# Kernel optimization log

Measured on AMD Instinct MI355X. Metric: run time of the kernel, lower is better.

Reference implementation:

```python
import jax, jax.numpy as jnp
import numpy as np

N = 131072      # number of RoIs (instances)
D = 1024        # in_channels
H = 1024        # hidden dim (hard-coded in module)
L = 4           # number of FPN levels / routed experts
STD = 0.01      # init std for all weights (biases zero)


def setup_inputs() -> dict:
    key = jax.random.key(0)
    k = jax.random.split(key, 5)
    x = jax.random.normal(k[0], (N, D), dtype=jnp.float32)
    levels = jax.random.randint(k[1], (N,), 0, L, dtype=jnp.int32)
    # Per-level MLP params, normal(std=0.01) weights, zero biases.
    W1 = jax.random.normal(k[2], (L, D, H), dtype=jnp.float32) * STD
    b1 = jnp.zeros((L, H), dtype=jnp.float32)
    W2 = jax.random.normal(k[3], (L, H, H), dtype=jnp.float32) * STD
    b2 = jnp.zeros((L, H), dtype=jnp.float32)
    W3 = jax.random.normal(k[4], (L, H, 1), dtype=jnp.float32) * STD
    b3 = jnp.zeros((L, 1), dtype=jnp.float32)
    return {"x": x, "levels": levels, "W1": W1, "b1": b1,
            "W2": W2, "b2": b2, "W3": W3, "b3": b3}


def reference(x, levels, W1, b1, W2, b2, W3, b3):
    # Hard-routed per-level 3-layer MLP (FC-ReLU x2 + FC), dropout in eval
    # mode (identity). Rows routed to level l get that level's MLP output;
    # implemented jit-compatibly with a fixed loop over the 4 levels and a
    # row mask instead of data-dependent gather/scatter.
    result = jnp.zeros((x.shape[0], 1), dtype=x.dtype)
    for lvl in range(L):
        h = jax.nn.relu(x @ W1[lvl] + b1[lvl])       # [N, H]
        h = jax.nn.relu(h @ W2[lvl] + b2[lvl])       # [N, H]
        out = h @ W3[lvl] + b3[lvl]                  # [N, 1]
        result = jnp.where((levels == lvl)[:, None], out, result)
    return result
```

## Files before the change

### kernel.cpp

```cpp
#include <hip/hip_runtime.h>

#define NROWS   131072
#define KDIM    1024
#define NLVL    4
#define SLOT_CAP 131584
#define NSB     1028

#define OFF_IDX  1024ull
#define OFF_PART (OFF_IDX + (size_t)SLOT_CAP * 4)
#define OFF_WT1  (OFF_PART + (size_t)SLOT_CAP * 64)
#define OFF_WT2  (OFF_WT1 + 8388608ull)
#define OFF_XBF  (OFF_WT2 + 8388608ull)
#define OFF_H1   (OFF_XBF + 268435456ull)

typedef __bf16 bf16x8 __attribute__((ext_vector_type(8)));
typedef float f32x4 __attribute__((ext_vector_type(4)));
typedef unsigned short u16x4 __attribute__((ext_vector_type(4)));

__device__ __forceinline__ unsigned short f2bf(float f) {
  unsigned int u = __float_as_uint(f);
  u += 0x7fffu + ((u >> 16) & 1u);
  return (unsigned short)(u >> 16);
}

__device__ __forceinline__ void gld_lds16(const void* g, void* l) {
  __builtin_amdgcn_global_load_lds(
      (const __attribute__((address_space(1))) void*)g,
      (__attribute__((address_space(3))) void*)l, 16, 0, 0);
}


__global__ void k_hist(const int* __restrict__ levels, int n, int* __restrict__ meta) {
  __shared__ int h[NLVL];
  if (threadIdx.x < NLVL) h[threadIdx.x] = 0;
  __syncthreads();
  for (int t = blockIdx.x * blockDim.x + threadIdx.x; t < n; t += gridDim.x * blockDim.x)
    atomicAdd(&h[levels[t]], 1);
  __syncthreads();
  if (threadIdx.x < NLVL) atomicAdd(&meta[threadIdx.x], h[threadIdx.x]);
}

__global__ void k_seg(int* meta) {
  if (threadIdx.x == 0 && blockIdx.x == 0) {
    int s = 0;
    for (int l = 0; l < NLVL; ++l) {
      int pc = (meta[l] + 127) & ~127;
      meta[8 + l] = s;
      meta[12 + l] = pc;
      s += pc;
    }
  }
}

__global__ void k_scatter(const int* __restrict__ levels, int n,
                          int* __restrict__ meta, int* __restrict__ idx) {
  __shared__ int h[NLVL], base[NLVL], cur[NLVL];
  int t = blockIdx.x * blockDim.x + threadIdx.x;
  if (threadIdx.x < NLVL) { h[threadIdx.x] = 0; cur[threadIdx.x] = 0; }
  __syncthreads();
  int lvl = 0;
  if (t < n) { lvl = levels[t]; atomicAdd(&h[lvl], 1); }
  __syncthreads();
  if (threadIdx.x < NLVL)
    base[threadIdx.x] = atomicAdd(&meta[4 + threadIdx.x], h[threadIdx.x]);
  __syncthreads();
  if (t < n) {
    int p = atomicAdd(&cur[lvl], 1);
    idx[meta[8 + lvl] + base[lvl] + p] = t;
  }
}

__global__ void k_cvt_x(const f32x4* __restrict__ x, u16x4* __restrict__ xb, int n4) {
  for (int t = blockIdx.x * blockDim.x + threadIdx.x; t < n4; t += gridDim.x * blockDim.x) {
    f32x4 v = x[t];
    u16x4 o;
    o[0] = f2bf(v[0]); o[1] = f2bf(v[1]); o[2] = f2bf(v[2]); o[3] = f2bf(v[3]);
    xb[t] = o;
  }
}

__global__ void k_twt(const float* __restrict__ W, unsigned short* __restrict__ Wt) {
  __shared__ float tile[32][33];
  int lvl = blockIdx.z;
  int k0 = blockIdx.x * 32, n0 = blockIdx.y * 32;
  int tx = threadIdx.x, ty = threadIdx.y;
  const float* Wp = W + (size_t)lvl * 1048576;
  unsigned short* Wtp = Wt + (size_t)lvl * 1048576;
#pragma unroll
  for (int i = 0; i < 4; ++i)
    tile[ty + i * 8][tx] = Wp[(size_t)(k0 + ty + i * 8) * 1024 + n0 + tx];
  __syncthreads();
#pragma unroll
  for (int i = 0; i < 4; ++i) {
    int nn = ty + i * 8;
    Wtp[(size_t)(n0 + nn) * 1024 + k0 + tx] = f2bf(tile[tx][nn]);
  }
}

template <int PASS>
__global__ __launch_bounds__(256) void k_gemm(
    const unsigned short* __restrict__ Asrc,
    const unsigned short* __restrict__ Wt,
    const float* __restrict__ bias,
    const float* __restrict__ w3,
    const int* __restrict__ meta,
    const int* __restrict__ idx,
    unsigned short* __restrict__ hout,
    float* __restrict__ partial) {
  const int bid = blockIdx.x;
  const int swz = (bid & 7) * NSB + (bid >> 3);
  const int nb = swz & 7;
  const int sb = swz >> 3;

  const int slotbase = sb * 128;
  if (slotbase >= meta[11] + meta[15]) return;
  int lvl;
  if      (slotbase < meta[9])  lvl = 0;
  else if (slotbase < meta[10]) lvl = 1;
  else if (slotbase < meta[11]) lvl = 2;
  else                          lvl = 3;

  const int tid = threadIdx.x;
  const int ln = tid & 63;
  const int w = tid >> 6;
  const int wm = w >> 1, wn = w & 1;

  __shared__ unsigned short Xl[128 * 64];
  __shared__ unsigned short Wl[128 * 64];

  const int srow = ln >> 3;
  const int schk = (ln & 7) ^ srow;
  const unsigned short* ag[4];
  const unsigned short* wg[4];
  unsigned short* xd[4];
  unsigned short* wd[4];
#pragma unroll
  for (int j = 0; j < 4; ++j) {
    int rloc = w * 32 + j * 8 + srow;
    int arow = (PASS == 1) ? idx[slotbase + rloc] : (slotbase + rloc);
    ag[j] = Asrc + (size_t)arow * 1024 + schk * 8;
    wg[j] = Wt + ((size_t)lvl * 1024 + nb * 128 + rloc) * 1024 + schk * 8;
    xd[j] = &Xl[(w * 32 + j * 8) * 64];
    wd[j] = &Wl[(w * 32 + j * 8) * 64];
  }

  const f32x4 vzero = {0.f, 0.f, 0.f, 0.f};
  f32x4 acc[4][4];
#pragma unroll
  for (int a = 0; a < 4; ++a)
#pragma unroll
    for (int b = 0; b < 4; ++b) acc[a][b] = vzero;

  const int rx = ln & 7;
  const int kg = ln >> 4;

  for (int k0 = 0; k0 < KDIM; k0 += 64) {
    __syncthreads();
#pragma unroll
    for (int j = 0; j < 4; ++j) gld_lds16(ag[j] + k0, xd[j]);
#pragma unroll
    for (int j = 0; j < 4; ++j) gld_lds16(wg[j] + k0, wd[j]);
    __syncthreads();
#pragma unroll
    for (int kk = 0; kk < 64; kk += 32) {
      const int chk = (((kk >> 3) + kg) ^ rx) * 8;
      bf16x8 aop[4], bop[4];
#pragma unroll
      for (int nf = 0; nf < 4; ++nf)
        aop[nf] = *(const bf16x8*)&Wl[(wn * 64 + nf * 16 + (ln & 15)) * 64 + chk];
#pragma unroll
      for (int mf = 0; mf < 4; ++mf)
        bop[mf] = *(const bf16x8*)&Xl[(wm * 64 + mf * 16 + (ln & 15)) * 64 + chk];
#pragma unroll
      for (int nf = 0; nf < 4; ++nf)
#pragma unroll
        for (int mf = 0; mf < 4; ++mf)
          acc[nf][mf] = __builtin_amdgcn_mfma_f32_16x16x32_bf16(aop[nf], bop[mf], acc[nf][mf], 0, 0, 0);
    }
  }

  const float* bv = bias + lvl * 1024;
  const int m_lo = ln & 15, n_lo = (ln >> 4) * 4;

  if (PASS == 1) {
#pragma unroll
    for (int nf = 0; nf < 4; ++nf) {
#pragma unroll
      for (int mf = 0; mf < 4; ++mf) {
        int slot = slotbase + wm * 64 + mf * 16 + m_lo;
        int col = nb * 128 + wn * 64 + nf * 16 + n_lo;
        f32x4 bb = *(const f32x4*)&bv[col];
        f32x4 v = acc[nf][mf];
        u16x4 o;
#pragma unroll
        for (int r = 0; r < 4; ++r) {
          float f = v[r] + bb[r];
          f = fmaxf(f, 0.f);
          o[r] = f2bf(f);
        }
        *(u16x4*)&hout[(size_t)slot * 1024 + col] = o;
      }
    }
  } else {
    const float* w3v = w3 + lvl * 1024;
    float ps[4] = {0.f, 0.f, 0.f, 0.f};
#pragma unroll
    for (int mf = 0; mf < 4; ++mf) {
#pragma unroll
      for (int nf = 0; nf < 4; ++nf) {
        int col = nb * 128 + wn * 64 + nf * 16 + n_lo;
        f32x4 bb = *(const f32x4*)&bv[col];
        f32x4 ww = *(const f32x4*)&w3v[col];
        f32x4 v = acc[nf][mf];
#pragma unroll
        for (int r = 0; r < 4; ++r) {
          float f = fmaxf(v[r] + bb[r], 0.f);
          ps[mf] += f * ww[r];
        }
      }
    }
#pragma unroll
    for (int mf = 0; mf < 4; ++mf) {
      float p = ps[mf];
      p += __shfl_xor(p, 16);
      p += __shfl_xor(p, 32);
      if (ln < 16) {
        int slot = slotbase + wm * 64 + mf * 16 + ln;
        partial[(size_t)slot * 16 + nb * 2 + wn] = p;
      }
    }
  }
}

__global__ void k_final(const int* __restrict__ meta, const int* __restrict__ idx,
                        const float* __restrict__ partial, const float* __restrict__ b3,
                        float* __restrict__ out) {
  int t = blockIdx.x * blockDim.x + threadIdx.x;
  int total = meta[11] + meta[15];
  if (t >= total) return;
  int lvl;
  if (t < meta[9]) lvl = 0;
  else if (t < meta[10]) lvl = 1;
  else if (t < meta[11]) lvl = 2;
  else lvl = 3;
  int local = t - meta[8 + lvl];
  if (local >= meta[lvl]) return;
  int row = idx[t];
  const float* pp = partial + (size_t)t * 16;
  float s = 0.f;
#pragma unroll
  for (int j = 0; j < 16; ++j) s += pp[j];
  out[row] = s + b3[lvl];
}

extern "C" void kernel_launch(void* const* d_in, const int* in_sizes, int n_in,
                              void* d_out, int out_size, void* d_ws, size_t ws_size,
                              hipStream_t stream) {
  const float* x      = (const float*)d_in[0];
  const int*   levels = (const int*)d_in[1];
  const float* W1     = (const float*)d_in[2];
  const float* b1     = (const float*)d_in[3];
  const float* W2     = (const float*)d_in[4];
  const float* b2     = (const float*)d_in[5];
  const float* W3     = (const float*)d_in[6];
  const float* b3     = (const float*)d_in[7];
  float* out = (float*)d_out;

  char* ws = (char*)d_ws;
  int* meta = (int*)ws;
  int* idx = (int*)(ws + OFF_IDX);
  float* partial = (float*)(ws + OFF_PART);
  unsigned short* Wt1 = (unsigned short*)(ws + OFF_WT1);
  unsigned short* Wt2 = (unsigned short*)(ws + OFF_WT2);
  unsigned short* xb  = (unsigned short*)(ws + OFF_XBF);
  unsigned short* h1  = (unsigned short*)(ws + OFF_H1);

  hipMemsetAsync(d_ws, 0, OFF_IDX + (size_t)SLOT_CAP * 4, stream);
  k_hist<<<256, 256, 0, stream>>>(levels, NROWS, meta);
  k_seg<<<1, 64, 0, stream>>>(meta);
  k_scatter<<<512, 256, 0, stream>>>(levels, NROWS, meta, idx);
  k_cvt_x<<<2048, 256, 0, stream>>>((const f32x4*)x, (u16x4*)xb, NROWS * (KDIM / 4));
  k_twt<<<dim3(32, 32, 4), dim3(32, 8), 0, stream>>>(W1, Wt1);
  k_twt<<<dim3(32, 32, 4), dim3(32, 8), 0, stream>>>(W2, Wt2);

  k_gemm<1><<<8 * NSB, 256, 0, stream>>>(xb, Wt1, b1, nullptr, meta, idx, h1, nullptr);
  k_gemm<2><<<8 * NSB, 256, 0, stream>>>(h1, Wt2, b2, W3, meta, idx, nullptr, partial);

  k_final<<<514, 256, 0, stream>>>(meta, idx, partial, b3, out);
}
```

Baseline: 960.1 us.

## Use 256x256 tiles with double-buffered 8-wave pipelined GEMM schedule

Enlarges the GEMM tile to 256x256 with 512 threads and a 128KB LDS double buffer, and moves level padding to 256 rows. The main loop is rewritten as an explicit software pipeline that interleaves async global-to-LDS loads with MFMA phases, using barriers, waitcnt and setprio. The aim is higher data reuse per load and overlap of memory traffic with matrix math. In exchange it uses heavy LDS and registers, lowering occupancy, and adds more padding rows per level.

```diff
diff --git a/kernel.cpp b/kernel.cpp
--- a/kernel.cpp
+++ b/kernel.cpp
@@ -3,8 +3,8 @@
 #define NROWS   131072
 #define KDIM    1024
 #define NLVL    4
-#define SLOT_CAP 131584
-#define NSB     1028
+#define SLOT_CAP 132096
+#define NSB     516
 
 #define OFF_IDX  1024ull
 #define OFF_PART (OFF_IDX + (size_t)SLOT_CAP * 4)
@@ -44,7 +44,7 @@
   if (threadIdx.x == 0 && blockIdx.x == 0) {
     int s = 0;
     for (int l = 0; l < NLVL; ++l) {
-      int pc = (meta[l] + 127) & ~127;
+      int pc = (meta[l] + 255) & ~255;
       meta[8 + l] = s;
       meta[12 + l] = pc;
       s += pc;
@@ -97,8 +97,23 @@
   }
 }
 
+#define BARR __builtin_amdgcn_s_barrier()
+#define WAIT_L  asm volatile("s_waitcnt lgkmcnt(0)" ::: "memory")
+#define WAIT_V6 asm volatile("s_waitcnt vmcnt(6) lgkmcnt(0)" ::: "memory")
+#define PRIO(x) __builtin_amdgcn_s_setprio(x)
+
+#define RD_W(pi,kk) { const char* p_ = lds + (((pi)*4 + (kk)) << 14) + offW0; \
+  wf[0] = *(const bf16x8*)(p_);        wf[1] = *(const bf16x8*)(p_ + 1024);  \
+  wf[2] = *(const bf16x8*)(p_ + 2048); wf[3] = *(const bf16x8*)(p_ + 3072); }
+#define RD_X(pi,kk,mh) { const char* p_ = lds + (((pi)*4 + 2 + (kk)) << 14) + offX0 + (mh)*4096; \
+  xf[0] = *(const bf16x8*)(p_);        xf[1] = *(const bf16x8*)(p_ + 1024);  \
+  xf[2] = *(const bf16x8*)(p_ + 2048); xf[3] = *(const bf16x8*)(p_ + 3072); }
+#define MMA(mh) { _Pragma("unroll") for (int nf_ = 0; nf_ < 4; ++nf_) { \
+  _Pragma("unroll") for (int j_ = 0; j_ < 4; ++j_) \
+    acc[nf_][(mh)*4 + j_] = __builtin_amdgcn_mfma_f32_16x16x32_bf16(wf[nf_], xf[j_], acc[nf_][(mh)*4 + j_], 0, 0, 0); } }
+
 template <int PASS>
-__global__ __launch_bounds__(256) void k_gemm(
+__global__ __launch_bounds__(512, 2) void k_gemm(
     const unsigned short* __restrict__ Asrc,
     const unsigned short* __restrict__ Wt,
     const float* __restrict__ bias,
@@ -107,12 +122,13 @@
     const int* __restrict__ idx,
     unsigned short* __restrict__ hout,
     float* __restrict__ partial) {
+  __shared__ __align__(16) char lds[131072];
+
   const int bid = blockIdx.x;
-  const int swz = (bid & 7) * NSB + (bid >> 3);
-  const int nb = swz & 7;
-  const int sb = swz >> 3;
-
-  const int slotbase = sb * 128;
+  const int swz = (bid & 7) * (NSB * 4 / 8) + (bid >> 3);
+  const int nb = swz & 3;
+  const int sb = swz >> 2;
+  const int slotbase = sb * 256;
   if (slotbase >= meta[11] + meta[15]) return;
   int lvl;
   if      (slotbase < meta[9])  lvl = 0;
@@ -121,112 +137,111 @@
   else                          lvl = 3;
 
   const int tid = threadIdx.x;
-  const int ln = tid & 63;
-  const int w = tid >> 6;
-  const int wm = w >> 1, wn = w & 1;
-
-  __shared__ unsigned short Xl[128 * 64];
-  __shared__ unsigned short Wl[128 * 64];
-
-  const int srow = ln >> 3;
-  const int schk = (ln & 7) ^ srow;
-  const unsigned short* ag[4];
-  const unsigned short* wg[4];
-  unsigned short* xd[4];
-  unsigned short* wd[4];
-#pragma unroll
-  for (int j = 0; j < 4; ++j) {
-    int rloc = w * 32 + j * 8 + srow;
-    int arow = (PASS == 1) ? idx[slotbase + rloc] : (slotbase + rloc);
-    ag[j] = Asrc + (size_t)arow * 1024 + schk * 8;
-    wg[j] = Wt + ((size_t)lvl * 1024 + nb * 128 + rloc) * 1024 + schk * 8;
-    xd[j] = &Xl[(w * 32 + j * 8) * 64];
-    wd[j] = &Wl[(w * 32 + j * 8) * 64];
-  }
+  const int ln  = tid & 63;
+  const int w   = tid >> 6;
+  const int wn  = w & 3;
+  const int wm  = w >> 2;
+  const int l15 = ln & 15;
+
+  const int rr0 = w * 16 + (ln >> 2);
+  const int cch = (ln & 3) ^ ((rr0 >> 1) & 3);
+  int ar0, ar1;
+  if (PASS == 1) { ar0 = idx[slotbase + rr0]; ar1 = idx[slotbase + rr0 + 128]; }
+  else           { ar0 = slotbase + rr0;      ar1 = slotbase + rr0 + 128; }
+  const char* xs0 = (const char*)Asrc + (size_t)ar0 * 2048 + cch * 16;
+  const char* xs1 = (const char*)Asrc + (size_t)ar1 * 2048 + cch * 16;
+  const char* wlv = (const char*)Wt + ((size_t)lvl << 21);
+  const char* ws0 = wlv + (size_t)(nb * 256 + rr0) * 2048 + cch * 16;
+  const char* ws1 = ws0 + 128 * 2048;
+
+  auto STG = [&](int t, int isX, int kkh) {
+    char* db = (char*)lds + (((t & 1) * 4 + isX * 2 + kkh) << 14) + (w << 10);
+    const char* s0 = isX ? xs0 : ws0;
+    const char* s1 = isX ? xs1 : ws1;
+    const int o = t * 128 + kkh * 64;
+    gld_lds16(s0 + o, db);
+    gld_lds16(s1 + o, db + 8192);
+  };
+
+  const int xorc  = ((ln >> 4) ^ ((l15 >> 1) & 3)) * 16;
+  const int offW0 = (wn * 64 + l15) * 64 + xorc;
+  const int offX0 = (wm * 128 + l15) * 64 + xorc;
 
   const f32x4 vzero = {0.f, 0.f, 0.f, 0.f};
-  f32x4 acc[4][4];
+  f32x4 acc[4][8];
 #pragma unroll
   for (int a = 0; a < 4; ++a)
 #pragma unroll
-    for (int b = 0; b < 4; ++b) acc[a][b] = vzero;
-
-  const int rx = ln & 7;
-  const int kg = ln >> 4;
-
-  for (int k0 = 0; k0 < KDIM; k0 += 64) {
-    __syncthreads();
-#pragma unroll
-    for (int j = 0; j < 4; ++j) gld_lds16(ag[j] + k0, xd[j]);
-#pragma unroll
-    for (int j = 0; j < 4; ++j) gld_lds16(wg[j] + k0, wd[j]);
-    __syncthreads();
-#pragma unroll
-    for (int kk = 0; kk < 64; kk += 32) {
-      const int chk = (((kk >> 3) + kg) ^ rx) * 8;
-      bf16x8 aop[4], bop[4];
-#pragma unroll
-      for (int nf = 0; nf < 4; ++nf)
-        aop[nf] = *(const bf16x8*)&Wl[(wn * 64 + nf * 16 + (ln & 15)) * 64 + chk];
-#pragma unroll
-      for (int mf = 0; mf < 4; ++mf)
-        bop[mf] = *(const bf16x8*)&Xl[(wm * 64 + mf * 16 + (ln & 15)) * 64 + chk];
-#pragma unroll
-      for (int nf = 0; nf < 4; ++nf)
-#pragma unroll
-        for (int mf = 0; mf < 4; ++mf)
-          acc[nf][mf] = __builtin_amdgcn_mfma_f32_16x16x32_bf16(aop[nf], bop[mf], acc[nf][mf], 0, 0, 0);
-    }
+    for (int b = 0; b < 8; ++b) acc[a][b] = vzero;
+  bf16x8 wf[4], xf[4];
+
+  STG(0, 0, 0); STG(0, 1, 0); STG(0, 0, 1); STG(0, 1, 1);
+  STG(1, 0, 0); STG(1, 1, 0); STG(1, 0, 1);
+  asm volatile("s_waitcnt vmcnt(6)" ::: "memory");
+  BARR;
+
+  for (int i = 0; i < 8; ++i) {
+    const int t0 = 2 * i, t1 = 2 * i + 1;
+    const bool g = (i < 7);
+    RD_W(0, 0); RD_X(0, 0, 0); STG(t1, 1, 1);
+    BARR; WAIT_L; PRIO(1); MMA(0); PRIO(0); BARR;
+    RD_X(0, 0, 1); if (g) STG(t0 + 2, 0, 0);
+    BARR; WAIT_L; PRIO(1); MMA(1); PRIO(0); BARR;
+    RD_W(0, 1); RD_X(0, 1, 0); if (g) STG(t0 + 2, 1, 0);
+    BARR; WAIT_L; PRIO(1); MMA(0); PRIO(0); BARR;
+    RD_X(0, 1, 1); if (g) STG(t0 + 2, 0, 1);
+    BARR; WAIT_V6; PRIO(1); MMA(1); PRIO(0); BARR;
+    RD_W(1, 0); RD_X(1, 0, 0); if (g) STG(t0 + 2, 1, 1);
+    BARR; WAIT_L; PRIO(1); MMA(0); PRIO(0); BARR;
+    RD_X(1, 0, 1); if (g) STG(t1 + 2, 0, 0);
+    BARR; WAIT_L; PRIO(1); MMA(1); PRIO(0); BARR;
+    RD_W(1, 1); RD_X(1, 1, 0); if (g) STG(t1 + 2, 1, 0);
+    BARR; WAIT_L; PRIO(1); MMA(0); PRIO(0); BARR;
+    RD_X(1, 1, 1); if (g) STG(t1 + 2, 0, 1);
+    BARR; WAIT_V6; PRIO(1); MMA(1); PRIO(0); BARR;
   }
 
   const float* bv = bias + lvl * 1024;
-  const int m_lo = ln & 15, n_lo = (ln >> 4) * 4;
+  const int n_lo = (ln >> 4) * 4;
 
   if (PASS == 1) {
 #pragma unroll
     for (int nf = 0; nf < 4; ++nf) {
 #pragma unroll
-      for (int mf = 0; mf < 4; ++mf) {
-        int slot = slotbase + wm * 64 + mf * 16 + m_lo;
-        int col = nb * 128 + wn * 64 + nf * 16 + n_lo;
+      for (int mf = 0; mf < 8; ++mf) {
+        int slot = slotbase + wm * 128 + mf * 16 + l15;
+        int col = nb * 256 + wn * 64 + nf * 16 + n_lo;
         f32x4 bb = *(const f32x4*)&bv[col];
         f32x4 v = acc[nf][mf];
         u16x4 o;
 #pragma unroll
-        for (int r = 0; r < 4; ++r) {
-          float f = v[r] + bb[r];
-          f = fmaxf(f, 0.f);
-          o[r] = f2bf(f);
-        }
+        for (int r = 0; r < 4; ++r) o[r] = f2bf(fmaxf(v[r] + bb[r], 0.f));
         *(u16x4*)&hout[(size_t)slot * 1024 + col] = o;
       }
     }
   } else {
     const float* w3v = w3 + lvl * 1024;
-    float ps[4] = {0.f, 0.f, 0.f, 0.f};
-#pragma unroll
-    for (int mf = 0; mf < 4; ++mf) {
+    float ps[8] = {0.f, 0.f, 0.f, 0.f, 0.f, 0.f, 0.f, 0.f};
+#pragma unroll
+    for (int mf = 0; mf < 8; ++mf) {
 #pragma unroll
       for (int nf = 0; nf < 4; ++nf) {
-        int col = nb * 128 + wn * 64 + nf * 16 + n_lo;
+        int col = nb * 256 + wn * 64 + nf * 16 + n_lo;
         f32x4 bb = *(const f32x4*)&bv[col];
         f32x4 ww = *(const f32x4*)&w3v[col];
         f32x4 v = acc[nf][mf];
 #pragma unroll
-        for (int r = 0; r < 4; ++r) {
-          float f = fmaxf(v[r] + bb[r], 0.f);
-          ps[mf] += f * ww[r];
-        }
+        for (int r = 0; r < 4; ++r) ps[mf] += fmaxf(v[r] + bb[r], 0.f) * ww[r];
       }
     }
 #pragma unroll
-    for (int mf = 0; mf < 4; ++mf) {
+    for (int mf = 0; mf < 8; ++mf) {
       float p = ps[mf];
       p += __shfl_xor(p, 16);
       p += __shfl_xor(p, 32);
       if (ln < 16) {
-        int slot = slotbase + wm * 64 + mf * 16 + ln;
-        partial[(size_t)slot * 16 + nb * 2 + wn] = p;
+        int slot = slotbase + wm * 128 + mf * 16 + ln;
+        partial[(size_t)slot * 16 + nb * 4 + wn] = p;
       }
     }
   }
@@ -283,8 +298,8 @@
   k_twt<<<dim3(32, 32, 4), dim3(32, 8), 0, stream>>>(W1, Wt1);
   k_twt<<<dim3(32, 32, 4), dim3(32, 8), 0, stream>>>(W2, Wt2);
 
-  k_gemm<1><<<8 * NSB, 256, 0, stream>>>(xb, Wt1, b1, nullptr, meta, idx, h1, nullptr);
-  k_gemm<2><<<8 * NSB, 256, 0, stream>>>(h1, Wt2, b2, W3, meta, idx, nullptr, partial);
-
-  k_final<<<514, 256, 0, stream>>>(meta, idx, partial, b3, out);
-}
+  k_gemm<1><<<NSB * 4, 512, 0, stream>>>(xb, Wt1, b1, nullptr, meta, idx, h1, nullptr);
+  k_gemm<2><<<NSB * 4, 512, 0, stream>>>(h1, Wt2, b2, W3, meta, idx, nullptr, partial);
+
+  k_final<<<516, 256, 0, stream>>>(meta, idx, partial, b3, out);
+}
```

New measurement: 811.8 us. 1.18x faster.
